# Optimization experiments

Measured on AMD Instinct MI355X. Metric: run time of the kernel, lower is better.

Reference implementation:

```python
import jax, jax.numpy as jnp
import numpy as np

L, D, H, DR, KF = 2, 256, 8, 64, 4   # n_layer, d_model, n_head, d_rpe, k_feedforward
B, S, T = 2, 256, 256
LN_EPS = 1e-5


def _ln(x, g, b):
    m = jnp.mean(x, -1, keepdims=True)
    v = jnp.mean((x - m) ** 2, -1, keepdims=True)
    return (x - m) * jax.lax.rsqrt(v + LN_EPS) * g + b


def _attn_rpe(q_in, kv_in, rpe, tgt_mask, wq, bq, wk, bk, wv, bv, wo, bo, wr, br):
    # RPE-biased multi-head cross attention: rpe -> (rpe_k, rpe_v) added per (src,tgt) pair.
    Bq, Sq, _ = q_in.shape
    Tk = kv_in.shape[1]
    Dh = D // H
    q = (q_in @ wq + bq).reshape(Bq, Sq, H, Dh)
    k = (kv_in @ wk + bk).reshape(Bq, Tk, H, Dh)
    v = (kv_in @ wv + bv).reshape(Bq, Tk, H, Dh)
    r = rpe @ wr + br                                   # [B,S,T,2D]
    rk, rv = jnp.split(r, 2, axis=-1)
    rk = rk.reshape(Bq, Sq, Tk, H, Dh)
    rv = rv.reshape(Bq, Sq, Tk, H, Dh)
    scale = 1.0 / np.sqrt(Dh).astype(np.float32)
    scores = (jnp.einsum('bshd,bthd->bhst', q, k)
              + jnp.einsum('bshd,bsthd->bhst', q, rk)) * scale
    scores = jnp.where(tgt_mask[:, None, None, :], -jnp.inf, scores)
    w = jax.nn.softmax(scores, axis=-1)                 # [B,H,S,T]
    out = (jnp.einsum('bhst,bthd->bshd', w, v)
           + jnp.einsum('bhst,bsthd->bshd', w, rv))
    return out.reshape(Bq, Sq, D) @ wo + bo


def _forward(src, tgt, rpe, src_padding_mask, tgt_padding_mask, p):
    for i in range(L):  # loop over n_layer (structurally distinct params)
        s2 = _ln(src, p['ln1_g'][i], p['ln1_b'][i])
        tn = _ln(tgt, p['lnt_g'][i], p['lnt_b'][i])
        a = _attn_rpe(s2, tn, rpe, tgt_padding_mask,
                      p['wq'][i], p['bq'][i], p['wk'][i], p['bk'][i],
                      p['wv'][i], p['bv'][i], p['wo'][i], p['bo'][i],
                      p['wr'][i], p['br'][i])
        src = src + a
        s2 = _ln(src, p['ln2_g'][i], p['ln2_b'][i])
        s2 = jax.nn.relu(s2 @ p['w1'][i] + p['b1'][i]) @ p['w2'][i] + p['b2'][i]
        src = src + s2
        src = jnp.where(src_padding_mask[:, :, None], 0.0, src)
    return src


def setup_inputs() -> dict:
    key = jax.random.key(0)
    ks = jax.random.split(key, 16)
    f = lambda k, shp: (0.02 * jax.random.normal(k, shp)).astype(jnp.float32)
    return {
        'src': jax.random.normal(ks[0], (B, S, D), jnp.float32),
        'tgt': jax.random.normal(ks[1], (B, T, D), jnp.float32),
        'rpe': jax.random.normal(ks[2], (B, S, T, DR), jnp.float32),
        'src_padding_mask': jax.random.bernoulli(ks[3], 0.05, (B, S)),
        'tgt_padding_mask': jax.random.bernoulli(ks[4], 0.1, (B, T)),
        'ln1_g': jnp.ones((L, D), jnp.float32), 'ln1_b': jnp.zeros((L, D), jnp.float32),
        'lnt_g': jnp.ones((L, D), jnp.float32), 'lnt_b': jnp.zeros((L, D), jnp.float32),
        'ln2_g': jnp.ones((L, D), jnp.float32), 'ln2_b': jnp.zeros((L, D), jnp.float32),
        'wq': f(ks[5], (L, D, D)), 'bq': jnp.zeros((L, D), jnp.float32),
        'wk': f(ks[6], (L, D, D)), 'bk': jnp.zeros((L, D), jnp.float32),
        'wv': f(ks[7], (L, D, D)), 'bv': jnp.zeros((L, D), jnp.float32),
        'wo': f(ks[8], (L, D, D)), 'bo': jnp.zeros((L, D), jnp.float32),
        'wr': f(ks[9], (L, DR, 2 * D)), 'br': jnp.zeros((L, 2 * D), jnp.float32),
        'w1': f(ks[10], (L, D, KF * D)), 'b1': jnp.zeros((L, KF * D), jnp.float32),
        'w2': f(ks[11], (L, KF * D, D)), 'b2': jnp.zeros((L, D), jnp.float32),
    }


def reference(src, tgt, rpe, src_padding_mask, tgt_padding_mask,
              ln1_g, ln1_b, lnt_g, lnt_b, ln2_g, ln2_b,
              wq, bq, wk, bk, wv, bv, wo, bo, wr, br, w1, b1, w2, b2):
    p = dict(ln1_g=ln1_g, ln1_b=ln1_b, lnt_g=lnt_g, lnt_b=lnt_b,
             ln2_g=ln2_g, ln2_b=ln2_b, wq=wq, bq=bq, wk=wk, bk=bk,
             wv=wv, bv=bv, wo=wo, bo=bo, wr=wr, br=br,
             w1=w1, b1=b1, w2=w2, b2=b2)
    return _forward(src, tgt, rpe, src_padding_mask, tgt_padding_mask, p)
```

## Files before the change

kernel.cpp:

```cpp
#include <hip/hip_runtime.h>
#include <math.h>

#define ROWS 512
#define DMODEL 256
#define NH 8
#define DH 32
#define NEG_INF -1e30f

__global__ __launch_bounds__(64) void ln_qt_kernel(
    const float* __restrict__ src, const float* __restrict__ tgt,
    const float* __restrict__ g1, const float* __restrict__ b1,
    const float* __restrict__ gt, const float* __restrict__ bt,
    const float* __restrict__ bo,
    float* __restrict__ S2, float* __restrict__ TNb, float* __restrict__ X)
{
  int row = blockIdx.x;
  const float* x; float* o; const float* g; const float* b;
  if (row < ROWS) { x = src + row * DMODEL; o = S2 + row * DMODEL; g = g1; b = b1; }
  else { int r = row - ROWS; x = tgt + r * DMODEL; o = TNb + r * DMODEL; g = gt; b = bt; }
  int lane = threadIdx.x;
  float4 v = ((const float4*)x)[lane];
  float s  = v.x + v.y + v.z + v.w;
  float ss = v.x*v.x + v.y*v.y + v.z*v.z + v.w*v.w;
#pragma unroll
  for (int off = 32; off >= 1; off >>= 1) {
    s  += __shfl_xor(s,  off);
    ss += __shfl_xor(ss, off);
  }
  float mean = s * (1.0f / 256.0f);
  float var  = ss * (1.0f / 256.0f) - mean * mean;
  float rstd = rsqrtf(var + 1e-5f);
  float4 gg = ((const float4*)g)[lane];
  float4 bb = ((const float4*)b)[lane];
  float4 ov;
  ov.x = (v.x - mean) * rstd * gg.x + bb.x;
  ov.y = (v.y - mean) * rstd * gg.y + bb.y;
  ov.z = (v.z - mean) * rstd * gg.z + bb.z;
  ov.w = (v.w - mean) * rstd * gg.w + bb.w;
  ((float4*)o)[lane] = ov;
  if (row < ROWS) {
    float4 bov = ((const float4*)bo)[lane];
    float4 xi;
    xi.x = v.x + bov.x; xi.y = v.y + bov.y; xi.z = v.z + bov.z; xi.w = v.w + bov.w;
    ((float4*)(X + row * DMODEL))[lane] = xi;
  }
}

__global__ __launch_bounds__(64) void ln2_kernel(
    const float* __restrict__ X, const float* __restrict__ g, const float* __restrict__ b,
    const float* __restrict__ b2, const int* __restrict__ smask,
    float* __restrict__ XN, float* __restrict__ outinit)
{
  int row = blockIdx.x;
  int lane = threadIdx.x;
  float4 v = ((const float4*)(X + row * DMODEL))[lane];
  float s  = v.x + v.y + v.z + v.w;
  float ss = v.x*v.x + v.y*v.y + v.z*v.z + v.w*v.w;
#pragma unroll
  for (int off = 32; off >= 1; off >>= 1) {
    s  += __shfl_xor(s,  off);
    ss += __shfl_xor(ss, off);
  }
  float mean = s * (1.0f / 256.0f);
  float var  = ss * (1.0f / 256.0f) - mean * mean;
  float rstd = rsqrtf(var + 1e-5f);
  float4 gg = ((const float4*)g)[lane];
  float4 bb = ((const float4*)b)[lane];
  float4 ov;
  ov.x = (v.x - mean) * rstd * gg.x + bb.x;
  ov.y = (v.y - mean) * rstd * gg.y + bb.y;
  ov.z = (v.z - mean) * rstd * gg.z + bb.z;
  ov.w = (v.w - mean) * rstd * gg.w + bb.w;
  ((float4*)(XN + row * DMODEL))[lane] = ov;
  float mm = (smask[row] != 0) ? 0.0f : 1.0f;
  float4 b2v = ((const float4*)b2)[lane];
  float4 oi;
  oi.x = mm * (v.x + b2v.x);
  oi.y = mm * (v.y + b2v.y);
  oi.z = mm * (v.z + b2v.z);
  oi.w = mm * (v.w + b2v.w);
  ((float4*)(outinit + row * DMODEL))[lane] = oi;
}

__device__ __forceinline__ void gemm_core32(
    const float* __restrict__ A, int lda,
    const float* __restrict__ Bw, int ldb,
    int kbeg, int kend, int m0, int n0,
    float acc[2][4])
{
  __shared__ float At[32][34];
  __shared__ float Bs[32][64];
  int tid = threadIdx.x;
  int tx = tid & 15, ty = tid >> 4;
  int r  = tid >> 3;
  int c4 = tid & 7;
  for (int kc = kbeg; kc < kend; kc += 32) {
    float4 a = *(const float4*)(A + (size_t)(m0 + r) * lda + kc + c4 * 4);
    const float* bp = Bw + (size_t)(kc + r) * ldb + n0;
    float4 b0 = *(const float4*)(bp + c4 * 4);
    float4 b1v = *(const float4*)(bp + 32 + c4 * 4);
    At[c4*4+0][r] = a.x; At[c4*4+1][r] = a.y; At[c4*4+2][r] = a.z; At[c4*4+3][r] = a.w;
    *(float4*)&Bs[r][c4*4]      = b0;
    *(float4*)&Bs[r][32 + c4*4] = b1v;
    __syncthreads();
#pragma unroll
    for (int k = 0; k < 32; ++k) {
      float2 av = *(const float2*)&At[k][ty * 2];
      float4 bv = *(const float4*)&Bs[k][tx * 4];
      acc[0][0] = fmaf(av.x, bv.x, acc[0][0]); acc[0][1] = fmaf(av.x, bv.y, acc[0][1]);
      acc[0][2] = fmaf(av.x, bv.z, acc[0][2]); acc[0][3] = fmaf(av.x, bv.w, acc[0][3]);
      acc[1][0] = fmaf(av.y, bv.x, acc[1][0]); acc[1][1] = fmaf(av.y, bv.y, acc[1][1]);
      acc[1][2] = fmaf(av.y, bv.z, acc[1][2]); acc[1][3] = fmaf(av.y, bv.w, acc[1][3]);
    }
    __syncthreads();
  }
}

__global__ __launch_bounds__(256) void qkv_kernel(
    const float* __restrict__ S2, const float* __restrict__ TNb,
    const float* __restrict__ wq, const float* __restrict__ wk, const float* __restrict__ wv,
    const float* __restrict__ bq, const float* __restrict__ bk, const float* __restrict__ bv,
    float* __restrict__ Qb, float* __restrict__ Kb, float* __restrict__ Vb)
{
  int z = blockIdx.z;
  const float* A    = (z == 0) ? S2 : TNb;
  const float* Bw   = (z == 0) ? wq : (z == 1) ? wk : wv;
  const float* bias = (z == 0) ? bq : (z == 1) ? bk : bv;
  int m0 = blockIdx.y * 32, n0 = blockIdx.x * 64;
  float acc[2][4] = {};
  gemm_core32(A, DMODEL, Bw, DMODEL, 0, DMODEL, m0, n0, acc);
  int tid = threadIdx.x, tx = tid & 15, ty = tid >> 4;
  int c0 = n0 + tx * 4;
  const float scale = 0.1767766952966369f;
#pragma unroll
  for (int i = 0; i < 2; ++i) {
    int m = m0 + ty * 2 + i;
    float4 r;
    r.x = acc[i][0] + bias[c0 + 0];
    r.y = acc[i][1] + bias[c0 + 1];
    r.z = acc[i][2] + bias[c0 + 2];
    r.w = acc[i][3] + bias[c0 + 3];
    if (z == 0) {
      r.x *= scale; r.y *= scale; r.z *= scale; r.w *= scale;
      *(float4*)&Qb[m * DMODEL + c0] = r;
    } else {
      int b = m >> 8, t = m & 255, h = c0 >> 5, d0 = c0 & 31;
      float* dst = ((z == 1) ? Kb : Vb) + (size_t)(b * NH + h) * 8192 + t * DH + d0;
      *(float4*)dst = r;
    }
  }
}

__global__ __launch_bounds__(256) void wo_kernel(
    const float* __restrict__ AO, const float* __restrict__ wo,
    float* __restrict__ X)
{
  int m0 = blockIdx.y * 32, n0 = blockIdx.x * 64;
  int kbeg = blockIdx.z * 128;
  float acc[2][4] = {};
  gemm_core32(AO, DMODEL, wo, DMODEL, kbeg, kbeg + 128, m0, n0, acc);
  int tid = threadIdx.x, tx = tid & 15, ty = tid >> 4;
  int c0 = n0 + tx * 4;
#pragma unroll
  for (int i = 0; i < 2; ++i) {
    int m = m0 + ty * 2 + i;
    atomicAdd(&X[m * DMODEL + c0 + 0], acc[i][0]);
    atomicAdd(&X[m * DMODEL + c0 + 1], acc[i][1]);
    atomicAdd(&X[m * DMODEL + c0 + 2], acc[i][2]);
    atomicAdd(&X[m * DMODEL + c0 + 3], acc[i][3]);
  }
}

__global__ __launch_bounds__(256) void ff1_kernel(
    const float* __restrict__ XN, const float* __restrict__ w1, const float* __restrict__ b1,
    float* __restrict__ H1)
{
  int m0 = blockIdx.y * 32, n0 = blockIdx.x * 64;
  float acc[2][4] = {};
  gemm_core32(XN, DMODEL, w1, 1024, 0, DMODEL, m0, n0, acc);
  int tid = threadIdx.x, tx = tid & 15, ty = tid >> 4;
  int c0 = n0 + tx * 4;
#pragma unroll
  for (int i = 0; i < 2; ++i) {
    int m = m0 + ty * 2 + i;
    float4 r;
    r.x = fmaxf(acc[i][0] + b1[c0 + 0], 0.0f);
    r.y = fmaxf(acc[i][1] + b1[c0 + 1], 0.0f);
    r.z = fmaxf(acc[i][2] + b1[c0 + 2], 0.0f);
    r.w = fmaxf(acc[i][3] + b1[c0 + 3], 0.0f);
    *(float4*)&H1[m * 1024 + c0] = r;
  }
}

__global__ __launch_bounds__(256) void ff2_kernel(
    const float* __restrict__ H1, const float* __restrict__ w2,
    const int* __restrict__ smask, float* __restrict__ outb)
{
  int m0 = blockIdx.y * 32, n0 = blockIdx.x * 64;
  int kbeg = blockIdx.z * 256;
  float acc[2][4] = {};
  gemm_core32(H1, 1024, w2, DMODEL, kbeg, kbeg + 256, m0, n0, acc);
  int tid = threadIdx.x, tx = tid & 15, ty = tid >> 4;
  int c0 = n0 + tx * 4;
#pragma unroll
  for (int i = 0; i < 2; ++i) {
    int m = m0 + ty * 2 + i;
    float mm = (smask[m] != 0) ? 0.0f : 1.0f;
    atomicAdd(&outb[m * DMODEL + c0 + 0], mm * acc[i][0]);
    atomicAdd(&outb[m * DMODEL + c0 + 1], mm * acc[i][1]);
    atomicAdd(&outb[m * DMODEL + c0 + 2], mm * acc[i][2]);
    atomicAdd(&outb[m * DMODEL + c0 + 3], mm * acc[i][3]);
  }
}

__global__ __launch_bounds__(256) void attn_kernel(
    const float* __restrict__ Qb, const float* __restrict__ Kb, const float* __restrict__ Vb,
    const float* __restrict__ rpe, const int* __restrict__ tmask,
    const float* __restrict__ wrl, const float* __restrict__ brl,
    float* __restrict__ AO)
{
  __shared__ float Ks[256][32];
  __shared__ float Vt[32][260];
  __shared__ float ps[4][256];
  __shared__ float qs[16][32];
  __shared__ float wks[5][32];
  __shared__ float wvs[5][32];
  int bid = blockIdx.x;
  int b = bid >> 7, h = (bid >> 4) & 7, s0 = (bid & 15) << 4;
  int tid = threadIdx.x;
  const float* Kp = Kb + (size_t)(b * NH + h) * 8192;
  const float* Vp = Vb + (size_t)(b * NH + h) * 8192;
  {
    int t = tid;
    const float4* kr = (const float4*)(Kp + t * DH);
    const float4* vr = (const float4*)(Vp + t * DH);
    int sw = t & 7;
#pragma unroll
    for (int c = 0; c < 8; ++c) {
      float4 k4 = kr[c];
      *(float4*)&Ks[t][(c ^ sw) * 4] = k4;
    }
#pragma unroll
    for (int c = 0; c < 8; ++c) {
      float4 v4 = vr[c];
      Vt[c*4+0][t] = v4.x; Vt[c*4+1][t] = v4.y; Vt[c*4+2][t] = v4.z; Vt[c*4+3][t] = v4.w;
    }
  }
  if (tid < 160) {
    int j = tid >> 5, d = tid & 31;
    wks[j][d] = (j < 4) ? wrl[j * 512 + h * DH + d]       : brl[h * DH + d];
    wvs[j][d] = (j < 4) ? wrl[j * 512 + 256 + h * DH + d] : brl[256 + h * DH + d];
  }
  if (tid >= 128) {
    int u = tid - 128;
    int rr = u >> 3, cc = u & 7;
    *(float4*)&qs[rr][cc*4] =
        *(const float4*)&Qb[(b * 256 + s0 + rr) * DMODEL + h * DH + cc * 4];
  }
  __syncthreads();

  int w = tid >> 6, lane = tid & 63;
  int msk[4];
#pragma unroll
  for (int it = 0; it < 4; ++it) msk[it] = tmask[b * 256 + it * 64 + lane];

  for (int i = 0; i < 4; ++i) {
    int sl = w * 4 + i;
    int s = s0 + sl;
    float4 q4[8];
#pragma unroll
    for (int c = 0; c < 8; ++c) q4[c] = *(const float4*)&qs[sl][c * 4];
    float qw[4]; float qbr = 0.0f;
#pragma unroll
    for (int j = 0; j < 4; ++j) {
      float t0 = 0;
#pragma unroll
      for (int c = 0; c < 8; ++c) {
        float4 wv4 = *(const float4*)&wks[j][c * 4];
        t0 += q4[c].x*wv4.x + q4[c].y*wv4.y + q4[c].z*wv4.z + q4[c].w*wv4.w;
      }
      qw[j] = t0;
    }
#pragma unroll
    for (int c = 0; c < 8; ++c) {
      float4 wv4 = *(const float4*)&wks[4][c * 4];
      qbr += q4[c].x*wv4.x + q4[c].y*wv4.y + q4[c].z*wv4.z + q4[c].w*wv4.w;
    }
    const float4* rp4 = (const float4*)(rpe + (size_t)(b * 256 + s) * 1024);
    float sc[4]; float4 rr[4];
#pragma unroll
    for (int it = 0; it < 4; ++it) {
      int t = it * 64 + lane;
      int sw = t & 7;
      float sv = 0;
#pragma unroll
      for (int c = 0; c < 8; ++c) {
        float4 k4 = *(const float4*)&Ks[t][(c ^ sw) * 4];
        sv = fmaf(q4[c].x, k4.x, sv); sv = fmaf(q4[c].y, k4.y, sv);
        sv = fmaf(q4[c].z, k4.z, sv); sv = fmaf(q4[c].w, k4.w, sv);
      }
      float4 rv = rp4[t];
      rr[it] = rv;
      sv += rv.x*qw[0] + rv.y*qw[1] + rv.z*qw[2] + rv.w*qw[3] + qbr;
      if (msk[it] != 0) sv = NEG_INF;
      sc[it] = sv;
    }
    float mval = fmaxf(fmaxf(sc[0], sc[1]), fmaxf(sc[2], sc[3]));
#pragma unroll
    for (int off = 32; off >= 1; off >>= 1) mval = fmaxf(mval, __shfl_xor(mval, off));
    float p[4], lsum = 0;
#pragma unroll
    for (int it = 0; it < 4; ++it) { p[it] = __expf(sc[it] - mval); lsum += p[it]; }
    float wj0 = 0, wj1 = 0, wj2 = 0, wj3 = 0;
#pragma unroll
    for (int it = 0; it < 4; ++it) {
      wj0 = fmaf(p[it], rr[it].x, wj0);
      wj1 = fmaf(p[it], rr[it].y, wj1);
      wj2 = fmaf(p[it], rr[it].z, wj2);
      wj3 = fmaf(p[it], rr[it].w, wj3);
    }
#pragma unroll
    for (int off = 32; off >= 1; off >>= 1) {
      lsum += __shfl_xor(lsum, off);
      wj0 += __shfl_xor(wj0, off);
      wj1 += __shfl_xor(wj1, off);
      wj2 += __shfl_xor(wj2, off);
      wj3 += __shfl_xor(wj3, off);
    }
#pragma unroll
    for (int it = 0; it < 4; ++it) ps[w][it * 64 + lane] = p[it];
    int g = lane >> 5, d = lane & 31;
    float o = 0;
#pragma unroll
    for (int n = 0; n < 32; ++n) {
      int t = g * 128 + n * 4;
      float4 p4 = *(const float4*)&ps[w][t];
      float4 v4 = *(const float4*)&Vt[d][t];
      o += p4.x*v4.x + p4.y*v4.y + p4.z*v4.z + p4.w*v4.w;
    }
    o += __shfl_xor(o, 32);
    float corr = wj0 * wvs[0][d] + wj1 * wvs[1][d] + wj2 * wvs[2][d] + wj3 * wvs[3][d];
    float oval = (o + corr) / lsum + wvs[4][d];
    if (lane < 32) AO[(b * 256 + s) * DMODEL + h * DH + d] = oval;
  }
}

extern "C" void kernel_launch(void* const* d_in, const int* in_sizes, int n_in,
                              void* d_out, int out_size, void* d_ws, size_t ws_size,
                              hipStream_t stream)
{
  const float* src  = (const float*)d_in[0];
  const float* tgt  = (const float*)d_in[1];
  const float* rpe  = (const float*)d_in[2];
  const int*   smask = (const int*)d_in[3];
  const int*   tmask = (const int*)d_in[4];
  const float* ln1g = (const float*)d_in[5];
  const float* ln1b = (const float*)d_in[6];
  const float* lntg = (const float*)d_in[7];
  const float* lntb = (const float*)d_in[8];
  const float* ln2g = (const float*)d_in[9];
  const float* ln2b = (const float*)d_in[10];
  const float* wq = (const float*)d_in[11];
  const float* bq = (const float*)d_in[12];
  const float* wk = (const float*)d_in[13];
  const float* bk = (const float*)d_in[14];
  const float* wv = (const float*)d_in[15];
  const float* bv = (const float*)d_in[16];
  const float* wo = (const float*)d_in[17];
  const float* bo = (const float*)d_in[18];
  const float* wr = (const float*)d_in[19];
  const float* br = (const float*)d_in[20];
  const float* w1 = (const float*)d_in[21];
  const float* b1 = (const float*)d_in[22];
  const float* w2 = (const float*)d_in[23];
  const float* b2 = (const float*)d_in[24];

  float* w    = (float*)d_ws;
  float* S2   = w;
  float* TNb  = w + 131072;
  float* Qb   = w + 262144;
  float* Kb   = w + 393216;
  float* Vb   = w + 524288;
  float* AO   = w + 655360;
  float* X    = w + 786432;
  float* XN   = w + 917504;
  float* SRC1 = w + 1048576;
  float* H1   = w + 1179648;

  for (int l = 0; l < 2; ++l) {
    const float* srcin = l ? SRC1 : src;
    float* outb = l ? (float*)d_out : SRC1;
    ln_qt_kernel<<<1024, 64, 0, stream>>>(srcin, tgt, ln1g + l*256, ln1b + l*256,
                                          lntg + l*256, lntb + l*256, bo + l*256,
                                          S2, TNb, X);
    qkv_kernel<<<dim3(4, 16, 3), 256, 0, stream>>>(S2, TNb,
                                                   wq + l*65536, wk + l*65536, wv + l*65536,
                                                   bq + l*256, bk + l*256, bv + l*256,
                                                   Qb, Kb, Vb);
    attn_kernel<<<256, 256, 0, stream>>>(Qb, Kb, Vb, rpe, tmask,
                                         wr + l*2048, br + l*512, AO);
    wo_kernel<<<dim3(4, 16, 2), 256, 0, stream>>>(AO, wo + l*65536, X);
    ln2_kernel<<<512, 64, 0, stream>>>(X, ln2g + l*256, ln2b + l*256, b2 + l*256,
                                       smask, XN, outb);
    ff1_kernel<<<dim3(16, 16), 256, 0, stream>>>(XN, w1 + l*262144, b1 + l*1024, H1);
    ff2_kernel<<<dim3(4, 16, 4), 256, 0, stream>>>(H1, w2 + l*262144, smask, outb);
  }
}
```

Measured before the change: 262.8 us.

## Fuse LayerNorms into the QKV and FF1 GEMM prologues

The standalone LayerNorm kernels are removed. LN1/LNt now run inside the QKV GEMM and LN2 inside the FF1 GEMM: each block normalizes its full 32-row A tile into shared memory before looping over weight tiles. This drops two launches per layer and the round trip of the normalized activations through global memory. In exchange, every column block recomputes the same row statistics and re-reads the full A rows, and the residual and output initialization writes are done only by the blockIdx.x==0 blocks.

After: 276.6 us. 5.2% more time.

```diff
diff --git a/kernel.cpp b/kernel.cpp
--- a/kernel.cpp
+++ b/kernel.cpp
@@ -1,85 +1,197 @@
 #include <hip/hip_runtime.h>
 #include <math.h>
 
-#define ROWS 512
-#define DMODEL 256
-#define NH 8
-#define DH 32
 #define NEG_INF -1e30f
 
-__global__ __launch_bounds__(64) void ln_qt_kernel(
-    const float* __restrict__ src, const float* __restrict__ tgt,
+__global__ __launch_bounds__(256) void qkv_ln_kernel(
+    const float* __restrict__ srcin, const float* __restrict__ tgt,
     const float* __restrict__ g1, const float* __restrict__ b1,
     const float* __restrict__ gt, const float* __restrict__ bt,
     const float* __restrict__ bo,
-    float* __restrict__ S2, float* __restrict__ TNb, float* __restrict__ X)
-{
-  int row = blockIdx.x;
-  const float* x; float* o; const float* g; const float* b;
-  if (row < ROWS) { x = src + row * DMODEL; o = S2 + row * DMODEL; g = g1; b = b1; }
-  else { int r = row - ROWS; x = tgt + r * DMODEL; o = TNb + r * DMODEL; g = gt; b = bt; }
-  int lane = threadIdx.x;
-  float4 v = ((const float4*)x)[lane];
-  float s  = v.x + v.y + v.z + v.w;
-  float ss = v.x*v.x + v.y*v.y + v.z*v.z + v.w*v.w;
-#pragma unroll
-  for (int off = 32; off >= 1; off >>= 1) {
+    const float* __restrict__ wq, const float* __restrict__ wk, const float* __restrict__ wv,
+    const float* __restrict__ bq, const float* __restrict__ bk, const float* __restrict__ bv,
+    float* __restrict__ Qb, float* __restrict__ Kb, float* __restrict__ Vb,
+    float* __restrict__ X)
+{
+  __shared__ float As[32][8][36];
+  __shared__ float Bs[32][64];
+  int z = blockIdx.z;
+  int m0 = blockIdx.y * 32, n0 = blockIdx.x * 64;
+  const float* Bw   = (z == 0) ? wq : (z == 1) ? wk : wv;
+  const float* bias = (z == 0) ? bq : (z == 1) ? bk : bv;
+  const float* g    = (z == 0) ? g1 : gt;
+  const float* be   = (z == 0) ? b1 : bt;
+  int tid = threadIdx.x;
+  int r = tid >> 3, c4 = tid & 7;
+  int row = m0 + r;
+  const float* arow = ((z == 0) ? srcin : tgt) + (size_t)row * 256 + c4 * 32;
+
+  float4 x[8];
+  float s = 0, ss = 0;
+#pragma unroll
+  for (int j = 0; j < 8; ++j) {
+    x[j] = ((const float4*)arow)[j];
+    s  += x[j].x + x[j].y + x[j].z + x[j].w;
+    ss += x[j].x*x[j].x + x[j].y*x[j].y + x[j].z*x[j].z + x[j].w*x[j].w;
+  }
+#pragma unroll
+  for (int off = 1; off < 8; off <<= 1) {
     s  += __shfl_xor(s,  off);
     ss += __shfl_xor(ss, off);
   }
   float mean = s * (1.0f / 256.0f);
   float var  = ss * (1.0f / 256.0f) - mean * mean;
   float rstd = rsqrtf(var + 1e-5f);
-  float4 gg = ((const float4*)g)[lane];
-  float4 bb = ((const float4*)b)[lane];
-  float4 ov;
-  ov.x = (v.x - mean) * rstd * gg.x + bb.x;
-  ov.y = (v.y - mean) * rstd * gg.y + bb.y;
-  ov.z = (v.z - mean) * rstd * gg.z + bb.z;
-  ov.w = (v.w - mean) * rstd * gg.w + bb.w;
-  ((float4*)o)[lane] = ov;
-  if (row < ROWS) {
-    float4 bov = ((const float4*)bo)[lane];
-    float4 xi;
-    xi.x = v.x + bov.x; xi.y = v.y + bov.y; xi.z = v.z + bov.z; xi.w = v.w + bov.w;
-    ((float4*)(X + row * DMODEL))[lane] = xi;
-  }
-}
-
-__global__ __launch_bounds__(64) void ln2_kernel(
-    const float* __restrict__ X, const float* __restrict__ g, const float* __restrict__ b,
+#pragma unroll
+  for (int j = 0; j < 8; ++j) {
+    float4 gg = ((const float4*)(g  + c4 * 32))[j];
+    float4 bb = ((const float4*)(be + c4 * 32))[j];
+    As[j*4+0][c4][r] = (x[j].x - mean) * rstd * gg.x + bb.x;
+    As[j*4+1][c4][r] = (x[j].y - mean) * rstd * gg.y + bb.y;
+    As[j*4+2][c4][r] = (x[j].z - mean) * rstd * gg.z + bb.z;
+    As[j*4+3][c4][r] = (x[j].w - mean) * rstd * gg.w + bb.w;
+  }
+  if (z == 0 && blockIdx.x == 0) {
+#pragma unroll
+    for (int j = 0; j < 8; ++j) {
+      float4 bo4 = ((const float4*)(bo + c4 * 32))[j];
+      float4 xi;
+      xi.x = x[j].x + bo4.x; xi.y = x[j].y + bo4.y;
+      xi.z = x[j].z + bo4.z; xi.w = x[j].w + bo4.w;
+      *(float4*)&X[(size_t)row * 256 + c4 * 32 + j * 4] = xi;
+    }
+  }
+  __syncthreads();
+
+  int tx = tid & 15, ty = tid >> 4;
+  float acc[2][4] = {};
+  for (int kc = 0; kc < 256; kc += 32) {
+    const float* bp = Bw + (size_t)(kc + r) * 256 + n0;
+    float4 b0  = *(const float4*)(bp + c4 * 4);
+    float4 b1v = *(const float4*)(bp + 32 + c4 * 4);
+    *(float4*)&Bs[r][c4 * 4]      = b0;
+    *(float4*)&Bs[r][32 + c4 * 4] = b1v;
+    __syncthreads();
+    int kcc = kc >> 5;
+#pragma unroll
+    for (int kk = 0; kk < 32; ++kk) {
+      float2 av = *(const float2*)&As[kk][kcc][ty * 2];
+      float4 bv = *(const float4*)&Bs[kk][tx * 4];
+      acc[0][0] = fmaf(av.x, bv.x, acc[0][0]); acc[0][1] = fmaf(av.x, bv.y, acc[0][1]);
+      acc[0][2] = fmaf(av.x, bv.z, acc[0][2]); acc[0][3] = fmaf(av.x, bv.w, acc[0][3]);
+      acc[1][0] = fmaf(av.y, bv.x, acc[1][0]); acc[1][1] = fmaf(av.y, bv.y, acc[1][1]);
+      acc[1][2] = fmaf(av.y, bv.z, acc[1][2]); acc[1][3] = fmaf(av.y, bv.w, acc[1][3]);
+    }
+    __syncthreads();
+  }
+
+  int c0 = n0 + tx * 4;
+  const float scale = 0.1767766952966369f;
+#pragma unroll
+  for (int i = 0; i < 2; ++i) {
+    int m = m0 + ty * 2 + i;
+    float4 rr;
+    rr.x = acc[i][0] + bias[c0 + 0];
+    rr.y = acc[i][1] + bias[c0 + 1];
+    rr.z = acc[i][2] + bias[c0 + 2];
+    rr.w = acc[i][3] + bias[c0 + 3];
+    if (z == 0) {
+      rr.x *= scale; rr.y *= scale; rr.z *= scale; rr.w *= scale;
+      *(float4*)&Qb[m * 256 + c0] = rr;
+    } else {
+      int b = m >> 8, t = m & 255, h = c0 >> 5, d0 = c0 & 31;
+      float* dst = ((z == 1) ? Kb : Vb) + (size_t)(b * 8 + h) * 8192 + t * 32 + d0;
+      *(float4*)dst = rr;
+    }
+  }
+}
+
+__global__ __launch_bounds__(256) void ff1_ln2_kernel(
+    const float* __restrict__ Xin,
+    const float* __restrict__ g2, const float* __restrict__ be2,
     const float* __restrict__ b2, const int* __restrict__ smask,
-    float* __restrict__ XN, float* __restrict__ outinit)
-{
-  int row = blockIdx.x;
-  int lane = threadIdx.x;
-  float4 v = ((const float4*)(X + row * DMODEL))[lane];
-  float s  = v.x + v.y + v.z + v.w;
-  float ss = v.x*v.x + v.y*v.y + v.z*v.z + v.w*v.w;
-#pragma unroll
-  for (int off = 32; off >= 1; off >>= 1) {
+    const float* __restrict__ w1, const float* __restrict__ b1,
+    float* __restrict__ H1, float* __restrict__ outb)
+{
+  __shared__ float As[32][8][36];
+  __shared__ float Bs[32][64];
+  int m0 = blockIdx.y * 32, n0 = blockIdx.x * 64;
+  int tid = threadIdx.x;
+  int r = tid >> 3, c4 = tid & 7;
+  int row = m0 + r;
+  const float* arow = Xin + (size_t)row * 256 + c4 * 32;
+
+  float4 x[8];
+  float s = 0, ss = 0;
+#pragma unroll
+  for (int j = 0; j < 8; ++j) {
+    x[j] = ((const float4*)arow)[j];
+    s  += x[j].x + x[j].y + x[j].z + x[j].w;
+    ss += x[j].x*x[j].x + x[j].y*x[j].y + x[j].z*x[j].z + x[j].w*x[j].w;
+  }
+#pragma unroll
+  for (int off = 1; off < 8; off <<= 1) {
     s  += __shfl_xor(s,  off);
     ss += __shfl_xor(ss, off);
   }
   float mean = s * (1.0f / 256.0f);
   float var  = ss * (1.0f / 256.0f) - mean * mean;
   float rstd = rsqrtf(var + 1e-5f);
-  float4 gg = ((const float4*)g)[lane];
-  float4 bb = ((const float4*)b)[lane];
-  float4 ov;
-  ov.x = (v.x - mean) * rstd * gg.x + bb.x;
-  ov.y = (v.y - mean) * rstd * gg.y + bb.y;
-  ov.z = (v.z - mean) * rstd * gg.z + bb.z;
-  ov.w = (v.w - mean) * rstd * gg.w + bb.w;
-  ((float4*)(XN + row * DMODEL))[lane] = ov;
-  float mm = (smask[row] != 0) ? 0.0f : 1.0f;
-  float4 b2v = ((const float4*)b2)[lane];
-  float4 oi;
-  oi.x = mm * (v.x + b2v.x);
-  oi.y = mm * (v.y + b2v.y);
-  oi.z = mm * (v.z + b2v.z);
-  oi.w = mm * (v.w + b2v.w);
-  ((float4*)(outinit + row * DMODEL))[lane] = oi;
+#pragma unroll
+  for (int j = 0; j < 8; ++j) {
+    float4 gg = ((const float4*)(g2  + c4 * 32))[j];
+    float4 bb = ((const float4*)(be2 + c4 * 32))[j];
+    As[j*4+0][c4][r] = (x[j].x - mean) * rstd * gg.x + bb.x;
+    As[j*4+1][c4][r] = (x[j].y - mean) * rstd * gg.y + bb.y;
+    As[j*4+2][c4][r] = (x[j].z - mean) * rstd * gg.z + bb.z;
+    As[j*4+3][c4][r] = (x[j].w - mean) * rstd * gg.w + bb.w;
+  }
+  if (blockIdx.x == 0) {
+    float mm = (smask[row] != 0) ? 0.0f : 1.0f;
+#pragma unroll
+    for (int j = 0; j < 8; ++j) {
+      float4 b24 = ((const float4*)(b2 + c4 * 32))[j];
+      float4 oi;
+      oi.x = mm * (x[j].x + b24.x); oi.y = mm * (x[j].y + b24.y);
+      oi.z = mm * (x[j].z + b24.z); oi.w = mm * (x[j].w + b24.w);
+      *(float4*)&outb[(size_t)row * 256 + c4 * 32 + j * 4] = oi;
+    }
+  }
+  __syncthreads();
+
+  int tx = tid & 15, ty = tid >> 4;
+  float acc[2][4] = {};
+  for (int kc = 0; kc < 256; kc += 32) {
+    const float* bp = w1 + (size_t)(kc + r) * 1024 + n0;
+    float4 b0  = *(const float4*)(bp + c4 * 4);
+    float4 b1v = *(const float4*)(bp + 32 + c4 * 4);
+    *(float4*)&Bs[r][c4 * 4]      = b0;
+    *(float4*)&Bs[r][32 + c4 * 4] = b1v;
+    __syncthreads();
+    int kcc = kc >> 5;
+#pragma unroll
+    for (int kk = 0; kk < 32; ++kk) {
+      float2 av = *(const float2*)&As[kk][kcc][ty * 2];
+      float4 bv = *(const float4*)&Bs[kk][tx * 4];
+      acc[0][0] = fmaf(av.x, bv.x, acc[0][0]); acc[0][1] = fmaf(av.x, bv.y, acc[0][1]);
+      acc[0][2] = fmaf(av.x, bv.z, acc[0][2]); acc[0][3] = fmaf(av.x, bv.w, acc[0][3]);
+      acc[1][0] = fmaf(av.y, bv.x, acc[1][0]); acc[1][1] = fmaf(av.y, bv.y, acc[1][1]);
+      acc[1][2] = fmaf(av.y, bv.z, acc[1][2]); acc[1][3] = fmaf(av.y, bv.w, acc[1][3]);
+    }
+    __syncthreads();
+  }
+
+  int c0 = n0 + tx * 4;
+#pragma unroll
+  for (int i = 0; i < 2; ++i) {
+    int m = m0 + ty * 2 + i;
+    float4 rr;
+    rr.x = fmaxf(acc[i][0] + b1[c0 + 0], 0.0f);
+    rr.y = fmaxf(acc[i][1] + b1[c0 + 1], 0.0f);
+    rr.z = fmaxf(acc[i][2] + b1[c0 + 2], 0.0f);
+    rr.w = fmaxf(acc[i][3] + b1[c0 + 3], 0.0f);
+    *(float4*)&H1[m * 1024 + c0] = rr;
+  }
 }
 
 __device__ __forceinline__ void gemm_core32(
@@ -116,41 +228,6 @@
   }
 }
 
-__global__ __launch_bounds__(256) void qkv_kernel(
-    const float* __restrict__ S2, const float* __restrict__ TNb,
-    const float* __restrict__ wq, const float* __restrict__ wk, const float* __restrict__ wv,
-    const float* __restrict__ bq, const float* __restrict__ bk, const float* __restrict__ bv,
-    float* __restrict__ Qb, float* __restrict__ Kb, float* __restrict__ Vb)
-{
-  int z = blockIdx.z;
-  const float* A    = (z == 0) ? S2 : TNb;
-  const float* Bw   = (z == 0) ? wq : (z == 1) ? wk : wv;
-  const float* bias = (z == 0) ? bq : (z == 1) ? bk : bv;
-  int m0 = blockIdx.y * 32, n0 = blockIdx.x * 64;
-  float acc[2][4] = {};
-  gemm_core32(A, DMODEL, Bw, DMODEL, 0, DMODEL, m0, n0, acc);
-  int tid = threadIdx.x, tx = tid & 15, ty = tid >> 4;
-  int c0 = n0 + tx * 4;
-  const float scale = 0.1767766952966369f;
-#pragma unroll
-  for (int i = 0; i < 2; ++i) {
-    int m = m0 + ty * 2 + i;
-    float4 r;
-    r.x = acc[i][0] + bias[c0 + 0];
-    r.y = acc[i][1] + bias[c0 + 1];
-    r.z = acc[i][2] + bias[c0 + 2];
-    r.w = acc[i][3] + bias[c0 + 3];
-    if (z == 0) {
-      r.x *= scale; r.y *= scale; r.z *= scale; r.w *= scale;
-      *(float4*)&Qb[m * DMODEL + c0] = r;
-    } else {
-      int b = m >> 8, t = m & 255, h = c0 >> 5, d0 = c0 & 31;
-      float* dst = ((z == 1) ? Kb : Vb) + (size_t)(b * NH + h) * 8192 + t * DH + d0;
-      *(float4*)dst = r;
-    }
-  }
-}
-
 __global__ __launch_bounds__(256) void wo_kernel(
     const float* __restrict__ AO, const float* __restrict__ wo,
     float* __restrict__ X)
@@ -158,37 +235,16 @@
   int m0 = blockIdx.y * 32, n0 = blockIdx.x * 64;
   int kbeg = blockIdx.z * 128;
   float acc[2][4] = {};
-  gemm_core32(AO, DMODEL, wo, DMODEL, kbeg, kbeg + 128, m0, n0, acc);
+  gemm_core32(AO, 256, wo, 256, kbeg, kbeg + 128, m0, n0, acc);
   int tid = threadIdx.x, tx = tid & 15, ty = tid >> 4;
   int c0 = n0 + tx * 4;
 #pragma unroll
   for (int i = 0; i < 2; ++i) {
     int m = m0 + ty * 2 + i;
-    atomicAdd(&X[m * DMODEL + c0 + 0], acc[i][0]);
-    atomicAdd(&X[m * DMODEL + c0 + 1], acc[i][1]);
-    atomicAdd(&X[m * DMODEL + c0 + 2], acc[i][2]);
-    atomicAdd(&X[m * DMODEL + c0 + 3], acc[i][3]);
-  }
-}
-
-__global__ __launch_bounds__(256) void ff1_kernel(
-    const float* __restrict__ XN, const float* __restrict__ w1, const float* __restrict__ b1,
-    float* __restrict__ H1)
-{
-  int m0 = blockIdx.y * 32, n0 = blockIdx.x * 64;
-  float acc[2][4] = {};
-  gemm_core32(XN, DMODEL, w1, 1024, 0, DMODEL, m0, n0, acc);
-  int tid = threadIdx.x, tx = tid & 15, ty = tid >> 4;
-  int c0 = n0 + tx * 4;
-#pragma unroll
-  for (int i = 0; i < 2; ++i) {
-    int m = m0 + ty * 2 + i;
-    float4 r;
-    r.x = fmaxf(acc[i][0] + b1[c0 + 0], 0.0f);
-    r.y = fmaxf(acc[i][1] + b1[c0 + 1], 0.0f);
-    r.z = fmaxf(acc[i][2] + b1[c0 + 2], 0.0f);
-    r.w = fmaxf(acc[i][3] + b1[c0 + 3], 0.0f);
-    *(float4*)&H1[m * 1024 + c0] = r;
+    atomicAdd(&X[m * 256 + c0 + 0], acc[i][0]);
+    atomicAdd(&X[m * 256 + c0 + 1], acc[i][1]);
+    atomicAdd(&X[m * 256 + c0 + 2], acc[i][2]);
+    atomicAdd(&X[m * 256 + c0 + 3], acc[i][3]);
   }
 }
 
@@ -199,17 +255,17 @@
   int m0 = blockIdx.y * 32, n0 = blockIdx.x * 64;
   int kbeg = blockIdx.z * 256;
   float acc[2][4] = {};
-  gemm_core32(H1, 1024, w2, DMODEL, kbeg, kbeg + 256, m0, n0, acc);
+  gemm_core32(H1, 1024, w2, 256, kbeg, kbeg + 256, m0, n0, acc);
   int tid = threadIdx.x, tx = tid & 15, ty = tid >> 4;
   int c0 = n0 + tx * 4;
 #pragma unroll
   for (int i = 0; i < 2; ++i) {
     int m = m0 + ty * 2 + i;
     float mm = (smask[m] != 0) ? 0.0f : 1.0f;
-    atomicAdd(&outb[m * DMODEL + c0 + 0], mm * acc[i][0]);
-    atomicAdd(&outb[m * DMODEL + c0 + 1], mm * acc[i][1]);
-    atomicAdd(&outb[m * DMODEL + c0 + 2], mm * acc[i][2]);
-    atomicAdd(&outb[m * DMODEL + c0 + 3], mm * acc[i][3]);
+    atomicAdd(&outb[m * 256 + c0 + 0], mm * acc[i][0]);
+    atomicAdd(&outb[m * 256 + c0 + 1], mm * acc[i][1]);
+    atomicAdd(&outb[m * 256 + c0 + 2], mm * acc[i][2]);
+    atomicAdd(&outb[m * 256 + c0 + 3], mm * acc[i][3]);
   }
 }
 
@@ -228,12 +284,12 @@
   int bid = blockIdx.x;
   int b = bid >> 7, h = (bid >> 4) & 7, s0 = (bid & 15) << 4;
   int tid = threadIdx.x;
-  const float* Kp = Kb + (size_t)(b * NH + h) * 8192;
-  const float* Vp = Vb + (size_t)(b * NH + h) * 8192;
+  const float* Kp = Kb + (size_t)(b * 8 + h) * 8192;
+  const float* Vp = Vb + (size_t)(b * 8 + h) * 8192;
   {
     int t = tid;
-    const float4* kr = (const float4*)(Kp + t * DH);
-    const float4* vr = (const float4*)(Vp + t * DH);
+    const float4* kr = (const float4*)(Kp + t * 32);
+    const float4* vr = (const float4*)(Vp + t * 32);
     int sw = t & 7;
 #pragma unroll
     for (int c = 0; c < 8; ++c) {
@@ -248,14 +304,14 @@
   }
   if (tid < 160) {
     int j = tid >> 5, d = tid & 31;
-    wks[j][d] = (j < 4) ? wrl[j * 512 + h * DH + d]       : brl[h * DH + d];
-    wvs[j][d] = (j < 4) ? wrl[j * 512 + 256 + h * DH + d] : brl[256 + h * DH + d];
+    wks[j][d] = (j < 4) ? wrl[j * 512 + h * 32 + d]       : brl[h * 32 + d];
+    wvs[j][d] = (j < 4) ? wrl[j * 512 + 256 + h * 32 + d] : brl[256 + h * 32 + d];
   }
   if (tid >= 128) {
     int u = tid - 128;
-    int rr = u >> 3, cc = u & 7;
-    *(float4*)&qs[rr][cc*4] =
-        *(const float4*)&Qb[(b * 256 + s0 + rr) * DMODEL + h * DH + cc * 4];
+    int rr2 = u >> 3, cc = u & 7;
+    *(float4*)&qs[rr2][cc*4] =
+        *(const float4*)&Qb[(b * 256 + s0 + rr2) * 256 + h * 32 + cc * 4];
   }
   __syncthreads();
 
@@ -341,7 +397,7 @@
     o += __shfl_xor(o, 32);
     float corr = wj0 * wvs[0][d] + wj1 * wvs[1][d] + wj2 * wvs[2][d] + wj3 * wvs[3][d];
     float oval = (o + corr) / lsum + wvs[4][d];
-    if (lane < 32) AO[(b * 256 + s) * DMODEL + h * DH + d] = oval;
+    if (lane < 32) AO[(b * 256 + s) * 256 + h * 32 + d] = oval;
   }
 }
 
@@ -375,34 +431,30 @@
   const float* w2 = (const float*)d_in[23];
   const float* b2 = (const float*)d_in[24];
 
-  float* w    = (float*)d_ws;
-  float* S2   = w;
-  float* TNb  = w + 131072;
-  float* Qb   = w + 262144;
-  float* Kb   = w + 393216;
-  float* Vb   = w + 524288;
-  float* AO   = w + 655360;
-  float* X    = w + 786432;
-  float* XN   = w + 917504;
-  float* SRC1 = w + 1048576;
-  float* H1   = w + 1179648;
+  float* ws   = (float*)d_ws;
+  float* Qb   = ws;
+  float* Kb   = ws + 131072;
+  float* Vb   = ws + 262144;
+  float* AO   = ws + 393216;
+  float* X    = ws + 524288;
+  float* SRC1 = ws + 655360;
+  float* H1   = ws + 786432;
 
   for (int l = 0; l < 2; ++l) {
     const float* srcin = l ? SRC1 : src;
     float* outb = l ? (float*)d_out : SRC1;
-    ln_qt_kernel<<<1024, 64, 0, stream>>>(srcin, tgt, ln1g + l*256, ln1b + l*256,
-                                          lntg + l*256, lntb + l*256, bo + l*256,
-                                          S2, TNb, X);
-    qkv_kernel<<<dim3(4, 16, 3), 256, 0, stream>>>(S2, TNb,
-                                                   wq + l*65536, wk + l*65536, wv + l*65536,
-                                                   bq + l*256, bk + l*256, bv + l*256,
-                                                   Qb, Kb, Vb);
+    qkv_ln_kernel<<<dim3(4, 16, 3), 256, 0, stream>>>(
+        srcin, tgt, ln1g + l*256, ln1b + l*256, lntg + l*256, lntb + l*256,
+        bo + l*256,
+        wq + l*65536, wk + l*65536, wv + l*65536,
+        bq + l*256, bk + l*256, bv + l*256,
+        Qb, Kb, Vb, X);
     attn_kernel<<<256, 256, 0, stream>>>(Qb, Kb, Vb, rpe, tmask,
                                          wr + l*2048, br + l*512, AO);
     wo_kernel<<<dim3(4, 16, 2), 256, 0, stream>>>(AO, wo + l*65536, X);
-    ln2_kernel<<<512, 64, 0, stream>>>(X, ln2g + l*256, ln2b + l*256, b2 + l*256,
-                                       smask, XN, outb);
-    ff1_kernel<<<dim3(16, 16), 256, 0, stream>>>(XN, w1 + l*262144, b1 + l*1024, H1);
+    ff1_ln2_kernel<<<dim3(16, 16), 256, 0, stream>>>(
+        X, ln2g + l*256, ln2b + l*256, b2 + l*256, smask,
+        w1 + l*262144, b1 + l*1024, H1, outb);
     ff2_kernel<<<dim3(4, 16, 4), 256, 0, stream>>>(H1, w2 + l*262144, smask, outb);
   }
 }
```
